# Performance work log

Hardware: AMD Instinct MI355X
Metric: run time of the kernel (lower is better)

Reference implementation:

```python
import jax, jax.numpy as jnp
import numpy as np

WINDOW_SHAPE = (12, 12, 32)  # (win_x, win_y, win_z)
GROUP_SIZE = 69
SHIFT = True


def setup_inputs() -> dict:
    rng = np.random.default_rng(0)
    Z, Y, X = 32, 512, 512
    batch_size = 8
    counts = [250000 + 37 * i + (i % 3) for i in range(batch_size)]  # non-multiples of GROUP_SIZE
    grid = Z * Y * X
    rows = []
    for b, n in enumerate(counts):
        lin = rng.choice(grid, size=n, replace=False)  # unique voxels per batch -> unique sort keys
        z = lin // (Y * X)
        y = (lin // X) % Y
        x = lin % X
        rows.append(np.stack([np.full(n, b), z, y, x], axis=1))
    coords = jnp.asarray(np.concatenate(rows, axis=0).astype(np.int32))
    return {"coords": coords, "batch_size": batch_size, "sparse_shape": (Z, Y, X)}


def reference(coords, batch_size, sparse_shape):
    g = GROUP_SIZE
    win_x, win_y, win_z = WINDOW_SHAPE
    sz, sy, sx = sparse_shape
    coords = coords.astype(jnp.int32)
    N = coords.shape[0]

    # ---- per-batch counts and (padded) start offsets (coords sorted by batch id) ----
    counts = jnp.bincount(coords[:, 0], length=batch_size).astype(jnp.int32)
    bs = jnp.concatenate([jnp.zeros(1, jnp.int32), jnp.cumsum(counts).astype(jnp.int32)])
    counts_p = ((counts + g - 1) // g) * g  # rounded up to multiple of group_size
    bsp = jnp.concatenate([jnp.zeros(1, jnp.int32), jnp.cumsum(counts_p).astype(jnp.int32)])
    Np = int(bsp[-1])  # padded total (eager; output length is data-dependent by construction)

    # ---- win2flat: original index -> padded position ----
    pb = coords[:, 0]  # batch of each point
    win2flat = jnp.arange(N, dtype=jnp.int32) + (bsp[:-1] - bs[:-1])[pb]

    # ---- flat2win: padded position -> original index (vectorized form of the torch loop) ----
    j = jnp.arange(Np, dtype=jnp.int32)
    b = (jnp.searchsorted(bsp, j, side='right') - 1).astype(jnp.int32)  # batch of padded pos
    off = bsp[b] - bs[b]
    num = counts[b]
    num_p = counts_p[b]
    r = num % g
    has_pad = num != num_p
    tail_start = jnp.where(has_pad, bsp[b + 1] - g + r, bsp[b + 1])
    in_tail = j >= tail_start
    multi_group = num_p != g
    val_multi = j - g - off                       # copy previous group's entries
    t = j - tail_start
    val_single = bs[b] + (t % jnp.maximum(num, 1))  # wrap-around repeat of batch elements
    flat2win = jnp.where(in_tail, jnp.where(multi_group, val_multi, val_single), j - off)

    # ---- window sort keys (win_version == 'v2') ----
    shift_x, shift_y, shift_z = (win_x // 2, win_y // 2, win_z // 2) if SHIFT else (0, 0, 0)
    mwx = int(np.ceil(sx / win_x) + 1)
    mwy = int(np.ceil(sy / win_y) + 1)
    mwz = int(np.ceil(sz / win_z) + 1)
    mps = mwx * mwy * mwz  # max windows per sample

    x = coords[:, 3] + shift_x
    y = coords[:, 2] + shift_y
    z = coords[:, 1] + shift_z
    wx, wy, wz = x // win_x, y // win_y, z // win_z
    cx, cy, cz = x % win_x, y % win_y, z % win_z

    bwi_x = coords[:, 0] * mps + wx * (mwy * mwz) + wy * mwz + wz
    bwi_y = coords[:, 0] * mps + wy * (mwx * mwz) + wx * mwz + wz

    vol = win_x * win_y * win_z
    vx = bwi_x * vol + cx * (win_y * win_z) + cy * win_z + cz
    vy = bwi_y * vol + cy * (win_x * win_z) + cx * win_z + cz

    x_map = jnp.argsort(vx).astype(jnp.int32)
    y_map = jnp.argsort(vy).astype(jnp.int32)

    return flat2win, win2flat, x_map, y_map
```

## Files before the change

### kernel.cpp

```cpp
#include <hip/hip_runtime.h>
#include <stdint.h>

#define G       69
#define BATCH   8
#define MPS     3872
#define VOL     4608
#define NBUK    1089
#define NB2     2178
#define B_WORDS 4096
#define STAGE   3072
#define BT      1024
#define CT      256
#define RT      512
#define NBLK    256

#define C_COUNTS 0
#define C_BS     8
#define C_CP     17
#define C_BSP    25
#define C_DONE   34

#define BSWZ(w) ((w) ^ (((w) >> 4) & 15))

__device__ __forceinline__ void keys_from_coord(int4 c, unsigned& kx, unsigned& ky) {
    int b  = c.x;
    int zz = c.y + 16;
    int yy = c.z + 6;
    int xx = c.w + 6;
    int wx = xx / 12, cx = xx - wx*12;
    int wy = yy / 12, cy = yy - wy*12;
    int wz = zz >> 5, cz = zz & 31;
    int bwx = b*MPS + wx*88 + wy*2 + wz;
    int bwy = b*MPS + wy*88 + wx*2 + wz;
    kx = (unsigned)(bwx*VOL + cx*384 + cy*32 + cz);
    ky = (unsigned)(bwy*VOL + cy*384 + cx*32 + cz);
}

__device__ __forceinline__ unsigned wave_iscan(unsigned x, int lane) {
    #pragma unroll
    for (int d = 1; d < 64; d <<= 1) {
        unsigned u = __shfl_up(x, d, 64);
        if (lane >= d) x += u;
    }
    return x;
}

__global__ __launch_bounds__(BT) void hist_kernel(const int4* __restrict__ coords, int N, int chunk,
                            int* __restrict__ ctrl, unsigned* __restrict__ histMat) {
    __shared__ unsigned h[NB2];
    __shared__ int hb[BATCH];
    int t = threadIdx.x, blk = blockIdx.x;
    for (int k = t; k < NB2; k += BT) h[k] = 0u;
    if (t < BATCH) hb[t] = 0;
    __syncthreads();
    int start = blk * chunk;
    int end   = min(start + chunk, N);
    int c0=0,c1=0,c2=0,c3=0,c4=0,c5=0,c6=0,c7=0;
    for (int i = start + t; i < end; i += BT) {
        int4 c = coords[i];
        int b = c.x;
        c0 += (b==0); c1 += (b==1); c2 += (b==2); c3 += (b==3);
        c4 += (b==4); c5 += (b==5); c6 += (b==6); c7 += (b==7);
        unsigned kx, ky;
        keys_from_coord(c, kx, ky);
        atomicAdd(&h[kx >> 17], 1u);
        atomicAdd(&h[NBUK + (ky >> 17)], 1u);
    }
    if (c0) atomicAdd(&hb[0],c0);  if (c1) atomicAdd(&hb[1],c1);
    if (c2) atomicAdd(&hb[2],c2);  if (c3) atomicAdd(&hb[3],c3);
    if (c4) atomicAdd(&hb[4],c4);  if (c5) atomicAdd(&hb[5],c5);
    if (c6) atomicAdd(&hb[6],c6);  if (c7) atomicAdd(&hb[7],c7);
    __syncthreads();
    for (int k = t; k < NB2; k += BT) histMat[(size_t)blk * NB2 + k] = h[k];
    if (t < BATCH && hb[t]) atomicAdd(&ctrl[C_COUNTS + t], hb[t]);
}

__global__ __launch_bounds__(CT) void colscan_kernel(int* __restrict__ ctrl,
                               unsigned* __restrict__ histMat,
                               unsigned* __restrict__ totals,
                               unsigned* __restrict__ recStart) {
    int t = threadIdx.x;
    int k = blockIdx.x * CT + t;
    if (k < NB2) {
        unsigned run = 0;
        for (int b = 0; b < NBLK; b += 16) {
            unsigned v[16];
            #pragma unroll
            for (int u = 0; u < 16; u++) v[u] = histMat[(size_t)(b+u)*NB2 + k];
            #pragma unroll
            for (int u = 0; u < 16; u++) { histMat[(size_t)(b+u)*NB2 + k] = run; run += v[u]; }
        }
        totals[k] = run;
    }
    __shared__ int s_last;
    __threadfence();
    __syncthreads();
    if (t == 0) {
        int d = atomicAdd(&ctrl[C_DONE], 1);
        s_last = (d == (int)gridDim.x - 1);
    }
    __syncthreads();
    if (!s_last) return;
    __threadfence();

    __shared__ unsigned warpsum[CT/64];
    __shared__ unsigned s_carry;
    int lane = t & 63, wid = t >> 6;
    if (t == 0) s_carry = 0u;
    __syncthreads();
    for (int base = 0; base < NB2; base += CT) {
        int idx = base + t;
        unsigned v = (idx < NB2) ? totals[idx] : 0u;
        unsigned x = wave_iscan(v, lane);
        if (lane == 63) warpsum[wid] = x;
        __syncthreads();
        if (wid == 0) {
            unsigned v2 = (lane < CT/64) ? warpsum[lane] : 0u;
            unsigned x2 = wave_iscan(v2, lane);
            if (lane < CT/64) warpsum[lane] = x2;
        }
        __syncthreads();
        unsigned excl = s_carry + (wid ? warpsum[wid-1] : 0u) + x - v;
        unsigned roundTot = warpsum[CT/64 - 1];
        if (idx < NB2) recStart[idx] = excl;
        __syncthreads();
        if (t == 0) s_carry += roundTot;
        __syncthreads();
    }
    if (t == 0) {
        recStart[NB2] = s_carry;
        int bs = 0, bsp = 0;
        ctrl[C_BS] = 0; ctrl[C_BSP] = 0;
        for (int b = 0; b < BATCH; b++) {
            int n  = ctrl[C_COUNTS + b];
            int np = ((n + G - 1) / G) * G;
            ctrl[C_CP + b] = np;
            bs += n; bsp += np;
            ctrl[C_BS + b + 1]  = bs;
            ctrl[C_BSP + b + 1] = bsp;
        }
    }
}

__global__ __launch_bounds__(BT) void bin_kernel(const int4* __restrict__ coords, int N, int chunk, int Np,
                           const int* __restrict__ ctrl,
                           const unsigned* __restrict__ recStart,
                           const unsigned* __restrict__ histMat,
                           uint2* __restrict__ rec,
                           int* __restrict__ w2f,
                           int* __restrict__ f2w) {
    __shared__ unsigned cur[NB2];
    __shared__ int s_off[BATCH];
    __shared__ int s_bs[BATCH+1], s_bsp[BATCH+1], s_cnt[BATCH], s_cp[BATCH];
    int t = threadIdx.x, blk = blockIdx.x;
    if (t < BATCH) {
        s_off[t] = ctrl[C_BSP+t] - ctrl[C_BS+t];
        s_cnt[t] = ctrl[C_COUNTS+t];
        s_cp[t]  = ctrl[C_CP+t];
    }
    if (t < BATCH+1) { s_bs[t] = ctrl[C_BS+t]; s_bsp[t] = ctrl[C_BSP+t]; }
    for (int k = t; k < NB2; k += BT)
        cur[k] = recStart[k] + histMat[(size_t)blk * NB2 + k];
    __syncthreads();
    int start = blk * chunk;
    int end   = min(start + chunk, N);
    for (int i = start + t; i < end; i += BT) {
        int4 c = coords[i];
        w2f[i] = i + s_off[c.x];
        unsigned kx, ky;
        keys_from_coord(c, kx, ky);
        unsigned px = atomicAdd(&cur[kx >> 17], 1u);
        rec[px] = make_uint2(kx, (unsigned)i);
        unsigned py = atomicAdd(&cur[NBUK + (ky >> 17)], 1u);
        rec[py] = make_uint2(ky, (unsigned)i);
    }
    int gs = (int)gridDim.x * BT;
    for (int j = blk*BT + t; j < Np; j += gs) {
        int b = 0;
        #pragma unroll
        for (int k = 1; k < BATCH; k++) b += (j >= s_bsp[k]);
        int off  = s_bsp[b] - s_bs[b];
        int num  = s_cnt[b], nump = s_cp[b];
        int r    = num % G;
        int tail_start = (num != nump) ? (s_bsp[b+1] - G + r) : s_bsp[b+1];
        int v;
        if (j < tail_start)       v = j - off;
        else if (nump != G)       v = j - G - off;
        else { int tt = j - tail_start; int m = num > 0 ? num : 1; v = s_bs[b] + tt % m; }
        f2w[j] = v;
    }
}

__global__ __launch_bounds__(RT) void rank_kernel(const uint2* __restrict__ rec,
                            const unsigned* __restrict__ recStart, int N,
                            int* __restrict__ xmap, int* __restrict__ ymap) {
    int b = blockIdx.x;
    unsigned start = recStart[b], end = recStart[b+1];
    int cnt = (int)(end - start);
    if (cnt == 0) return;
    int map = (b >= NBUK);
    __shared__ unsigned bits[B_WORDS];
    __shared__ unsigned short pref[B_WORDS];
    __shared__ uint2 stage[STAGE];
    __shared__ unsigned wsum[RT/64];
    int t = threadIdx.x;
    #pragma unroll
    for (int k = 0; k < B_WORDS/RT; k++) bits[t + RT*k] = 0u;
    __syncthreads();
    for (int j = t; j < cnt; j += RT) {
        uint2 r = rec[start + j];
        if (j < STAGE) stage[j] = r;
        unsigned local = r.x & 131071u;
        atomicOr(&bits[BSWZ(local >> 5)], 1u << (local & 31));
    }
    __syncthreads();
    int base = t * (B_WORDS/RT);
    unsigned w[B_WORDS/RT];
    unsigned s = 0;
    #pragma unroll
    for (int k = 0; k < B_WORDS/RT; k++) { w[k] = bits[BSWZ(base + k)]; s += __popc(w[k]); }
    int lane = t & 63, wid = t >> 6;
    unsigned x = wave_iscan(s, lane);
    if (lane == 63) wsum[wid] = x;
    __syncthreads();
    unsigned add = 0;
    #pragma unroll
    for (int q = 0; q < RT/64 - 1; q++) add += (wid > q) ? wsum[q] : 0u;
    unsigned excl = add + x - s;
    #pragma unroll
    for (int k = 0; k < B_WORDS/RT; k++) {
        pref[BSWZ(base + k)] = (unsigned short)excl;
        excl += __popc(w[k]);
    }
    __syncthreads();
    int* __restrict__ out = map ? ymap : xmap;
    unsigned rankBase = start - (map ? (unsigned)N : 0u);
    for (int j = t; j < cnt; j += RT) {
        uint2 r = (j < STAGE) ? stage[j] : rec[start + j];
        unsigned local = r.x & 131071u;
        unsigned wd = local >> 5, bt = local & 31u;
        unsigned sw = BSWZ(wd);
        unsigned rank = rankBase + (unsigned)pref[sw] + __popc(bits[sw] & ((1u << bt) - 1u));
        out[rank] = (int)r.y;
    }
}

extern "C" void kernel_launch(void* const* d_in, const int* in_sizes, int n_in,
                              void* d_out, int out_size, void* d_ws, size_t ws_size,
                              hipStream_t stream) {
    const int* coords = (const int*)d_in[0];
    int N  = in_sizes[0] / 4;
    int Np = out_size - 3 * N;
    int chunk = (N + NBLK - 1) / NBLK;

    char* ws = (char*)d_ws;
    int*      ctrl     = (int*)(ws + 0);
    unsigned* totals   = (unsigned*)(ws + 256);
    unsigned* recStart = (unsigned*)(ws + 8968);
    unsigned* histMat  = (unsigned*)(ws + 17696);
    uint2*    rec      = (uint2*)(ws + 2247968);

    int* out  = (int*)d_out;
    int* f2w  = out;
    int* w2f  = out + Np;
    int* xmap = out + Np + N;
    int* ymap = out + Np + 2*N;

    hipMemsetAsync(ctrl, 0, 256, stream);

    hist_kernel<<<NBLK, BT, 0, stream>>>((const int4*)coords, N, chunk, ctrl, histMat);
    colscan_kernel<<<(NB2 + CT - 1)/CT, CT, 0, stream>>>(ctrl, histMat, totals, recStart);
    bin_kernel<<<NBLK, BT, 0, stream>>>((const int4*)coords, N, chunk, Np, ctrl, recStart, histMat, rec, w2f, f2w);
    rank_kernel<<<NB2, RT, 0, stream>>>(rec, recStart, N, xmap, ymap);
}
```

Baseline: 156.7 us.

## Fuse hist, column scan and binning into one cooperative kernel with register-cached keys

Merges the histogram, column-scan/prefix and scatter kernels into a single cooperative launch separated by grid.sync, and keeps the computed sort keys in registers between phases so coords are not reloaded and keys not recomputed. This is meant to remove two kernel launches and the second pass over the input. The register cache assumes each block's chunk is at most 8*1024 elements, which fails silently for larger N. Cooperative launch also requires all 256 blocks of 1024 threads to be co-resident, and the grid barriers add their own cost.

```diff
diff --git a/kernel.cpp b/kernel.cpp
--- a/kernel.cpp
+++ b/kernel.cpp
@@ -1,24 +1,26 @@
 #include <hip/hip_runtime.h>
+#include <hip/hip_cooperative_groups.h>
 #include <stdint.h>
+
+namespace cg = cooperative_groups;
 
 #define G       69
 #define BATCH   8
 #define MPS     3872
 #define VOL     4608
+#define VOLMPS  17842176
 #define NBUK    1089
 #define NB2     2178
 #define B_WORDS 4096
 #define STAGE   3072
-#define BT      1024
-#define CT      256
+#define FT      1024
+#define FBLK    256
 #define RT      512
-#define NBLK    256
 
 #define C_COUNTS 0
 #define C_BS     8
 #define C_CP     17
 #define C_BSP    25
-#define C_DONE   34
 
 #define BSWZ(w) ((w) ^ (((w) >> 4) & 15))
 
@@ -45,137 +47,137 @@
     return x;
 }
 
-__global__ __launch_bounds__(BT) void hist_kernel(const int4* __restrict__ coords, int N, int chunk,
-                            int* __restrict__ ctrl, unsigned* __restrict__ histMat) {
+__global__ __launch_bounds__(FT) void fused_kernel(const int4* __restrict__ coords,
+                             int N, int chunk, int Np,
+                             int* __restrict__ ctrl,
+                             unsigned* __restrict__ histMat,
+                             unsigned* __restrict__ totals,
+                             unsigned* __restrict__ recStart,
+                             uint2* __restrict__ rec,
+                             int* __restrict__ w2f,
+                             int* __restrict__ f2w) {
+    cg::grid_group grid = cg::this_grid();
     __shared__ unsigned h[NB2];
     __shared__ int hb[BATCH];
+    __shared__ unsigned warpsum[FT/64];
+    __shared__ unsigned s_carry;
+    __shared__ int s_off[BATCH];
+    __shared__ int s_bs[BATCH+1], s_bsp[BATCH+1], s_cnt[BATCH], s_cp[BATCH];
+
     int t = threadIdx.x, blk = blockIdx.x;
-    for (int k = t; k < NB2; k += BT) h[k] = 0u;
+    int lane = t & 63, wid = t >> 6;
+
+    for (int k = t; k < NB2; k += FT) h[k] = 0u;
     if (t < BATCH) hb[t] = 0;
     __syncthreads();
     int start = blk * chunk;
     int end   = min(start + chunk, N);
+    unsigned kxA[8], kyA[8];
     int c0=0,c1=0,c2=0,c3=0,c4=0,c5=0,c6=0,c7=0;
-    for (int i = start + t; i < end; i += BT) {
-        int4 c = coords[i];
-        int b = c.x;
-        c0 += (b==0); c1 += (b==1); c2 += (b==2); c3 += (b==3);
-        c4 += (b==4); c5 += (b==5); c6 += (b==6); c7 += (b==7);
-        unsigned kx, ky;
-        keys_from_coord(c, kx, ky);
-        atomicAdd(&h[kx >> 17], 1u);
-        atomicAdd(&h[NBUK + (ky >> 17)], 1u);
+    #pragma unroll
+    for (int it = 0; it < 8; ++it) {
+        int i = start + it*FT + t;
+        kxA[it] = 0u; kyA[it] = 0u;
+        if (i < end) {
+            int4 c = coords[i];
+            int b = c.x;
+            c0 += (b==0); c1 += (b==1); c2 += (b==2); c3 += (b==3);
+            c4 += (b==4); c5 += (b==5); c6 += (b==6); c7 += (b==7);
+            unsigned kx, ky;
+            keys_from_coord(c, kx, ky);
+            kxA[it] = kx; kyA[it] = ky;
+            atomicAdd(&h[kx >> 17], 1u);
+            atomicAdd(&h[NBUK + (ky >> 17)], 1u);
+        }
     }
     if (c0) atomicAdd(&hb[0],c0);  if (c1) atomicAdd(&hb[1],c1);
     if (c2) atomicAdd(&hb[2],c2);  if (c3) atomicAdd(&hb[3],c3);
     if (c4) atomicAdd(&hb[4],c4);  if (c5) atomicAdd(&hb[5],c5);
     if (c6) atomicAdd(&hb[6],c6);  if (c7) atomicAdd(&hb[7],c7);
     __syncthreads();
-    for (int k = t; k < NB2; k += BT) histMat[(size_t)blk * NB2 + k] = h[k];
+    for (int k = t; k < NB2; k += FT) histMat[(size_t)blk * NB2 + k] = h[k];
     if (t < BATCH && hb[t]) atomicAdd(&ctrl[C_COUNTS + t], hb[t]);
-}
-
-__global__ __launch_bounds__(CT) void colscan_kernel(int* __restrict__ ctrl,
-                               unsigned* __restrict__ histMat,
-                               unsigned* __restrict__ totals,
-                               unsigned* __restrict__ recStart) {
-    int t = threadIdx.x;
-    int k = blockIdx.x * CT + t;
-    if (k < NB2) {
+
+    grid.sync();
+
+    int gt = blk * FT + t;
+    if (gt < NB2) {
         unsigned run = 0;
-        for (int b = 0; b < NBLK; b += 16) {
+        for (int b = 0; b < FBLK; b += 16) {
             unsigned v[16];
             #pragma unroll
-            for (int u = 0; u < 16; u++) v[u] = histMat[(size_t)(b+u)*NB2 + k];
+            for (int u = 0; u < 16; u++) v[u] = histMat[(size_t)(b+u)*NB2 + gt];
             #pragma unroll
-            for (int u = 0; u < 16; u++) { histMat[(size_t)(b+u)*NB2 + k] = run; run += v[u]; }
-        }
-        totals[k] = run;
-    }
-    __shared__ int s_last;
-    __threadfence();
-    __syncthreads();
-    if (t == 0) {
-        int d = atomicAdd(&ctrl[C_DONE], 1);
-        s_last = (d == (int)gridDim.x - 1);
-    }
-    __syncthreads();
-    if (!s_last) return;
-    __threadfence();
-
-    __shared__ unsigned warpsum[CT/64];
-    __shared__ unsigned s_carry;
-    int lane = t & 63, wid = t >> 6;
-    if (t == 0) s_carry = 0u;
-    __syncthreads();
-    for (int base = 0; base < NB2; base += CT) {
-        int idx = base + t;
-        unsigned v = (idx < NB2) ? totals[idx] : 0u;
-        unsigned x = wave_iscan(v, lane);
-        if (lane == 63) warpsum[wid] = x;
+            for (int u = 0; u < 16; u++) { histMat[(size_t)(b+u)*NB2 + gt] = run; run += v[u]; }
+        }
+        totals[gt] = run;
+    }
+
+    grid.sync();
+
+    if (blk == 0) {
+        if (t == 0) s_carry = 0u;
         __syncthreads();
-        if (wid == 0) {
-            unsigned v2 = (lane < CT/64) ? warpsum[lane] : 0u;
-            unsigned x2 = wave_iscan(v2, lane);
-            if (lane < CT/64) warpsum[lane] = x2;
-        }
-        __syncthreads();
-        unsigned excl = s_carry + (wid ? warpsum[wid-1] : 0u) + x - v;
-        unsigned roundTot = warpsum[CT/64 - 1];
-        if (idx < NB2) recStart[idx] = excl;
-        __syncthreads();
-        if (t == 0) s_carry += roundTot;
-        __syncthreads();
-    }
-    if (t == 0) {
-        recStart[NB2] = s_carry;
-        int bs = 0, bsp = 0;
-        ctrl[C_BS] = 0; ctrl[C_BSP] = 0;
-        for (int b = 0; b < BATCH; b++) {
-            int n  = ctrl[C_COUNTS + b];
-            int np = ((n + G - 1) / G) * G;
-            ctrl[C_CP + b] = np;
-            bs += n; bsp += np;
-            ctrl[C_BS + b + 1]  = bs;
-            ctrl[C_BSP + b + 1] = bsp;
-        }
-    }
-}
-
-__global__ __launch_bounds__(BT) void bin_kernel(const int4* __restrict__ coords, int N, int chunk, int Np,
-                           const int* __restrict__ ctrl,
-                           const unsigned* __restrict__ recStart,
-                           const unsigned* __restrict__ histMat,
-                           uint2* __restrict__ rec,
-                           int* __restrict__ w2f,
-                           int* __restrict__ f2w) {
-    __shared__ unsigned cur[NB2];
-    __shared__ int s_off[BATCH];
-    __shared__ int s_bs[BATCH+1], s_bsp[BATCH+1], s_cnt[BATCH], s_cp[BATCH];
-    int t = threadIdx.x, blk = blockIdx.x;
+        for (int base = 0; base < NB2; base += FT) {
+            int idx = base + t;
+            unsigned v = (idx < NB2) ? totals[idx] : 0u;
+            unsigned x = wave_iscan(v, lane);
+            if (lane == 63) warpsum[wid] = x;
+            __syncthreads();
+            if (wid == 0) {
+                unsigned v2 = (lane < FT/64) ? warpsum[lane] : 0u;
+                unsigned x2 = wave_iscan(v2, lane);
+                if (lane < FT/64) warpsum[lane] = x2;
+            }
+            __syncthreads();
+            unsigned excl = s_carry + (wid ? warpsum[wid-1] : 0u) + x - v;
+            unsigned roundTot = warpsum[FT/64 - 1];
+            if (idx < NB2) recStart[idx] = excl;
+            __syncthreads();
+            if (t == 0) s_carry += roundTot;
+            __syncthreads();
+        }
+        if (t == 0) {
+            recStart[NB2] = s_carry;
+            int bs = 0, bsp = 0;
+            ctrl[C_BS] = 0; ctrl[C_BSP] = 0;
+            for (int b = 0; b < BATCH; b++) {
+                int n  = ctrl[C_COUNTS + b];
+                int np = ((n + G - 1) / G) * G;
+                ctrl[C_CP + b] = np;
+                bs += n; bsp += np;
+                ctrl[C_BS + b + 1]  = bs;
+                ctrl[C_BSP + b + 1] = bsp;
+            }
+        }
+    }
+
+    grid.sync();
+
     if (t < BATCH) {
         s_off[t] = ctrl[C_BSP+t] - ctrl[C_BS+t];
         s_cnt[t] = ctrl[C_COUNTS+t];
         s_cp[t]  = ctrl[C_CP+t];
     }
     if (t < BATCH+1) { s_bs[t] = ctrl[C_BS+t]; s_bsp[t] = ctrl[C_BSP+t]; }
-    for (int k = t; k < NB2; k += BT)
-        cur[k] = recStart[k] + histMat[(size_t)blk * NB2 + k];
-    __syncthreads();
-    int start = blk * chunk;
-    int end   = min(start + chunk, N);
-    for (int i = start + t; i < end; i += BT) {
-        int4 c = coords[i];
-        w2f[i] = i + s_off[c.x];
-        unsigned kx, ky;
-        keys_from_coord(c, kx, ky);
-        unsigned px = atomicAdd(&cur[kx >> 17], 1u);
-        rec[px] = make_uint2(kx, (unsigned)i);
-        unsigned py = atomicAdd(&cur[NBUK + (ky >> 17)], 1u);
-        rec[py] = make_uint2(ky, (unsigned)i);
-    }
-    int gs = (int)gridDim.x * BT;
-    for (int j = blk*BT + t; j < Np; j += gs) {
+    for (int k = t; k < NB2; k += FT)
+        h[k] = recStart[k] + histMat[(size_t)blk * NB2 + k];
+    __syncthreads();
+    #pragma unroll
+    for (int it = 0; it < 8; ++it) {
+        int i = start + it*FT + t;
+        if (i < end) {
+            unsigned kx = kxA[it], ky = kyA[it];
+            int b = (int)(kx / VOLMPS);
+            w2f[i] = i + s_off[b];
+            unsigned px = atomicAdd(&h[kx >> 17], 1u);
+            rec[px] = make_uint2(kx, (unsigned)i);
+            unsigned py = atomicAdd(&h[NBUK + (ky >> 17)], 1u);
+            rec[py] = make_uint2(ky, (unsigned)i);
+        }
+    }
+    int gs = FBLK * FT;
+    for (int j = blk*FT + t; j < Np; j += gs) {
         int b = 0;
         #pragma unroll
         for (int k = 1; k < BATCH; k++) b += (j >= s_bsp[k]);
@@ -248,10 +250,10 @@
 extern "C" void kernel_launch(void* const* d_in, const int* in_sizes, int n_in,
                               void* d_out, int out_size, void* d_ws, size_t ws_size,
                               hipStream_t stream) {
-    const int* coords = (const int*)d_in[0];
+    const int4* coords = (const int4*)d_in[0];
     int N  = in_sizes[0] / 4;
     int Np = out_size - 3 * N;
-    int chunk = (N + NBLK - 1) / NBLK;
+    int chunk = (N + FBLK - 1) / FBLK;
 
     char* ws = (char*)d_ws;
     int*      ctrl     = (int*)(ws + 0);
@@ -268,8 +270,10 @@
 
     hipMemsetAsync(ctrl, 0, 256, stream);
 
-    hist_kernel<<<NBLK, BT, 0, stream>>>((const int4*)coords, N, chunk, ctrl, histMat);
-    colscan_kernel<<<(NB2 + CT - 1)/CT, CT, 0, stream>>>(ctrl, histMat, totals, recStart);
-    bin_kernel<<<NBLK, BT, 0, stream>>>((const int4*)coords, N, chunk, Np, ctrl, recStart, histMat, rec, w2f, f2w);
+    void* args[] = { (void*)&coords, (void*)&N, (void*)&chunk, (void*)&Np,
+                     (void*)&ctrl, (void*)&histMat, (void*)&totals, (void*)&recStart,
+                     (void*)&rec, (void*)&w2f, (void*)&f2w };
+    hipLaunchCooperativeKernel((const void*)fused_kernel, dim3(FBLK), dim3(FT),
+                               args, 0, stream);
     rank_kernel<<<NB2, RT, 0, stream>>>(rec, recStart, N, xmap, ymap);
 }
```

After: 263.5 us. +68.2%, slower.
